# Performance work log

Hardware: AMD Instinct MI355X
Metric: run time of the kernel (lower is better)

Reference implementation:

```python
import jax, jax.numpy as jnp
import numpy as np

B, L, S, H = 2, 256, 384, 768
Tc, Dc = 16, 50
WV, WD = 20000, 100
CV = 128
NEG = -1e30


def _lstm_scan(x, Wih, Whh, bih, bhh):
    # x: [N, T, D] -> hs: [N, T, Hc]; torch LSTM gate order i,f,g,o
    N = x.shape[0]
    Hc = Whh.shape[1]
    h0 = jnp.zeros((N, Hc), x.dtype)

    def step(carry, xt):
        h, c = carry
        g = xt @ Wih.T + h @ Whh.T + bih + bhh  # [N, 4Hc]
        i, f, gg, o = jnp.split(g, 4, axis=-1)
        i = jax.nn.sigmoid(i)
        f = jax.nn.sigmoid(f)
        gg = jnp.tanh(gg)
        o = jax.nn.sigmoid(o)
        c = f * c + i * gg
        h = o * jnp.tanh(c)
        return (h, c), h

    _, hs = jax.lax.scan(step, (h0, h0), jnp.swapaxes(x, 0, 1))
    return jnp.swapaxes(hs, 0, 1)


def setup_inputs() -> dict:
    key = jax.random.key(0)
    ks = jax.random.split(key, 10)
    bert_emb = jax.random.normal(ks[0], (B, S, H), jnp.float32)
    pieces2word = jax.random.randint(ks[1], (B, L, S), 0, 2, jnp.int32)
    word_ids = jax.random.randint(ks[2], (B, L), 0, WV, jnp.int32)
    char_count = jax.random.randint(ks[3], (B, L), 1, Tc + 1, jnp.int32)
    char_ids = jax.random.randint(ks[4], (B, L, Tc), 0, CV, jnp.int32)
    # mask consistent with ragged char lengths (first char_count positions valid)
    token_masks_char = (jnp.arange(Tc)[None, None, :] < char_count[..., None]).astype(jnp.int32)
    word_table = jax.random.normal(ks[5], (WV, WD), jnp.float32) * 0.02
    char_table = jax.random.normal(ks[6], (CV, Dc), jnp.float32) * 0.02
    sc = 1.0 / np.sqrt(Dc)

    def lstm_w(k):
        a, b, c, d = jax.random.split(k, 4)
        return (jax.random.uniform(a, (4 * Dc, Dc), jnp.float32, -sc, sc),
                jax.random.uniform(b, (4 * Dc, Dc), jnp.float32, -sc, sc),
                jax.random.uniform(c, (4 * Dc,), jnp.float32, -sc, sc),
                jax.random.uniform(d, (4 * Dc,), jnp.float32, -sc, sc))

    Wih_f, Whh_f, bih_f, bhh_f = lstm_w(ks[7])
    Wih_b, Whh_b, bih_b, bhh_b = lstm_w(ks[8])
    return dict(bert_emb=bert_emb, pieces2word=pieces2word, word_ids=word_ids,
                char_count=char_count, char_ids=char_ids, token_masks_char=token_masks_char,
                word_table=word_table, char_table=char_table,
                Wih_f=Wih_f, Whh_f=Whh_f, bih_f=bih_f, bhh_f=bhh_f,
                Wih_b=Wih_b, Whh_b=Whh_b, bih_b=bih_b, bhh_b=bhh_b)


def reference(bert_emb, pieces2word, word_ids, char_count, char_ids, token_masks_char,
              word_table, char_table, Wih_f, Whh_f, bih_f, bhh_f, Wih_b, Whh_b, bih_b, bhh_b):
    # --- piece2word max pool (expand + masked_fill(min) + max over pieces) ---
    minv = jnp.min(bert_emb)
    # [B, L, S, H] intermediate, as in the original expand
    masked = jnp.where(pieces2word[..., None] != 0, bert_emb[:, None, :, :], minv)
    word_reps = jnp.max(masked, axis=2)  # [B, L, H]
    # dropouts are identity in eval mode

    # --- word embedding lookup ---
    word_embed = word_table[word_ids]  # [B, L, WD]

    # --- char bi-LSTM with packed-sequence semantics ---
    lens = jnp.maximum(char_count.reshape(-1), 1)  # char_count[char_count==0]=1
    x = char_table[char_ids.reshape(B * L, Tc)]  # [N, Tc, Dc]
    h_fwd = _lstm_scan(x, Wih_f, Whh_f, bih_f, bhh_f)
    # reverse each sequence within its valid length for the backward direction
    t = jnp.arange(Tc)[None, :]
    idx = jnp.where(t < lens[:, None], lens[:, None] - 1 - t, t)  # [N, Tc]
    x_rev = jnp.take_along_axis(x, idx[..., None], axis=1)
    h_bwd = _lstm_scan(x_rev, Wih_b, Whh_b, bih_b, bhh_b)
    h_bwd = jnp.take_along_axis(h_bwd, idx[..., None], axis=1)  # back to original order
    h = jnp.concatenate([h_fwd, h_bwd], axis=-1)  # [N, Tc, 2*Dc]
    valid = (t < lens[:, None])[..., None]
    h = jnp.where(valid, h, 0.0)  # pad_packed_sequence zero-pads beyond length
    h = h.reshape(B, L, Tc, 2 * Dc)

    # --- combine(..., 'max'): masked max over ragged char groups ---
    m = jnp.where(token_masks_char[..., None] == 0, NEG, 0.0)
    sup = jnp.max(m + h, axis=2)  # [B, L, 2*Dc]
    sup = jnp.where(sup == NEG, 0.0, sup)

    return jnp.concatenate([word_reps, word_embed, sup], axis=-1)  # [B, L, H+WD+2*Dc]
```

## Files before the change

kernel.cpp:

```cpp
#include <hip/hip_runtime.h>
#include <float.h>

#define Bb 2
#define Ll 256
#define Ss 384
#define Hh 768
#define Tc 16
#define Dc 50
#define WD 100
#define CV 128
#define NG 200
#define OUTC 968


__device__ inline float tanh_fast(float x) {
    float e = __expf(2.f * x);
    return 1.f - 2.f / (e + 1.f);
}
__device__ inline float sigmoid_fast(float x) {
    return 1.f / (1.f + __expf(-x));
}


__global__ __launch_bounds__(256) void prep_kernel(
        const float* __restrict__ bert, const float* __restrict__ char_table,
        const float* __restrict__ Wih_f, const float* __restrict__ bih_f, const float* __restrict__ bhh_f,
        const float* __restrict__ Wih_b, const float* __restrict__ bih_b, const float* __restrict__ bhh_b,
        const int* __restrict__ word_ids, const float* __restrict__ word_table,
        float* __restrict__ minp, float* __restrict__ xpt, float* __restrict__ out) {
    int blk = blockIdx.x, tid = threadIdx.x;
    if (blk < 256) {
        const int n = Bb * Ss * Hh;
        float m = FLT_MAX;
        for (int i = blk * 256 + tid; i < n; i += 256 * 256) m = fminf(m, bert[i]);
        #pragma unroll
        for (int off = 32; off; off >>= 1) m = fminf(m, __shfl_down(m, off, 64));
        __shared__ float red[4];
        if ((tid & 63) == 0) red[tid >> 6] = m;
        __syncthreads();
        if (tid == 0) minp[blk] = fminf(fminf(red[0], red[1]), fminf(red[2], red[3]));
    } else if (blk < 272) {
        int idx = blk - 256;
        int dir = idx >> 3, c0 = (idx & 7) * 16;
        const float* Wih = dir ? Wih_b : Wih_f;
        const float* bih = dir ? bih_b : bih_f;
        const float* bhh = dir ? bhh_b : bhh_f;
        __shared__ float ct[16][Dc];
        for (int e = tid; e < 16 * Dc; e += 256)
            ((float*)ct)[e] = char_table[c0 * Dc + e];
        __syncthreads();
        if (tid < NG) {
            float w[Dc];
            #pragma unroll
            for (int j = 0; j < Dc; j++) w[j] = Wih[tid * Dc + j];
            float bias = bih[tid] + bhh[tid];
            for (int cid = 0; cid < 16; cid++) {
                float a = bias;
                #pragma unroll
                for (int j = 0; j < Dc; j++) a += w[j] * ct[cid][j];
                xpt[(dir * CV + c0 + cid) * NG + tid] = a;
            }
        }
    } else {
        for (int i = (blk - 272) * 256 + tid; i < Bb * Ll * WD; i += 64 * 256) {
            int bl = i / WD, d = i - bl * WD;
            out[(size_t)bl * OUTC + Hh + d] = word_table[(size_t)word_ids[bl] * WD + d];
        }
    }
}


#define LT 8

__global__ __launch_bounds__(256) void word_kernel(
        const float* __restrict__ bert, const int* __restrict__ p2w,
        const float* __restrict__ minp, float* __restrict__ out) {
    int tid = threadIdx.x;
    __shared__ float sminv;
    __shared__ float sacc[4][LT][128];
    if (tid < 64) {
        float m = fminf(fminf(minp[tid], minp[tid + 64]),
                        fminf(minp[tid + 128], minp[tid + 192]));
        #pragma unroll
        for (int off = 32; off; off >>= 1) m = fminf(m, __shfl_down(m, off, 64));
        if (tid == 0) sminv = m;
    }
    int blk = blockIdx.x;
    int hc = blk % 6;
    int lt = (blk / 6) & 31;
    int b  = blk / 192;
    int l0 = lt * LT;
    int w    = tid >> 6;
    int lane = tid & 63;

    const float2* bb2 = (const float2*)(bert + (size_t)b * Ss * Hh + hc * 128);
    const int*    pm  = p2w + ((size_t)b * Ll + l0) * Ss;

    float2 acc[LT];
    #pragma unroll
    for (int r = 0; r < LT; r++) { acc[r].x = -FLT_MAX; acc[r].y = -FLT_MAX; }

    int s0 = w * 96;
    for (int s = s0; s < s0 + 96; s += 4) {
        float2 v0 = bb2[(size_t)(s + 0) * 384 + lane];
        float2 v1 = bb2[(size_t)(s + 1) * 384 + lane];
        float2 v2 = bb2[(size_t)(s + 2) * 384 + lane];
        float2 v3 = bb2[(size_t)(s + 3) * 384 + lane];
        #pragma unroll
        for (int r = 0; r < LT; r++) {
            const int* pr = pm + r * Ss + s;
            if (pr[0]) { acc[r].x = fmaxf(acc[r].x, v0.x); acc[r].y = fmaxf(acc[r].y, v0.y); }
            if (pr[1]) { acc[r].x = fmaxf(acc[r].x, v1.x); acc[r].y = fmaxf(acc[r].y, v1.y); }
            if (pr[2]) { acc[r].x = fmaxf(acc[r].x, v2.x); acc[r].y = fmaxf(acc[r].y, v2.y); }
            if (pr[3]) { acc[r].x = fmaxf(acc[r].x, v3.x); acc[r].y = fmaxf(acc[r].y, v3.y); }
        }
    }
    #pragma unroll
    for (int r = 0; r < LT; r++)
        *(float2*)&sacc[w][r][lane * 2] = acc[r];
    __syncthreads();

    float mv = sminv;
    #pragma unroll
    for (int e = tid; e < LT * 128; e += 256) {
        int r = e >> 7, c = e & 127;
        float m0 = fmaxf(sacc[0][r][c], sacc[1][r][c]);
        float m1 = fmaxf(sacc[2][r][c], sacc[3][r][c]);
        float m  = fmaxf(m0, m1);
        if (m == -FLT_MAX) m = mv;
        out[((size_t)(b * Ll + l0 + r)) * OUTC + hc * 128 + c] = m;
    }
}


__global__ __launch_bounds__(256) void lstm_kernel(
        const int* __restrict__ char_ids, const int* __restrict__ char_count,
        const float* __restrict__ Whh_f, const float* __restrict__ Whh_b,
        const float* __restrict__ xpt, float* __restrict__ out) {
    int n = blockIdx.x, dir = blockIdx.y, tid = threadIdx.x;
    const float* Whh = dir ? Whh_b : Whh_f;

    __shared__ float xg[Tc][NG];
    __shared__ float gs[NG];
    __shared__ __align__(16) float hs[52];
    __shared__ int scid[Tc];

    int len = char_count[n];
    if (len < 1) len = 1;
    if (tid < Tc) {
        int t = tid;
        int st = dir ? (t < len ? len - 1 - t : t) : t;
        scid[t] = char_ids[n * Tc + st];
    }
    if (tid < 52) hs[tid] = 0.f;
    __syncthreads();

    for (int e = tid; e < Tc * NG; e += 256) {
        int t = e / NG, g = e - t * NG;
        xg[t][g] = xpt[(dir * CV + scid[t]) * NG + g];
    }
    float w[52];
    if (tid < NG) {
        #pragma unroll
        for (int j = 0; j < Dc; j++) w[j] = Whh[tid * Dc + j];
        w[50] = 0.f; w[51] = 0.f;
    }
    __syncthreads();

    float c = 0.f, maxv = -FLT_MAX;
    for (int t = 0; t < Tc; t++) {
        if (tid < NG) {
            float g = xg[t][tid];
            #pragma unroll
            for (int j = 0; j < 52; j += 4) {
                float4 hv = *(const float4*)&hs[j];
                g += hv.x * w[j] + hv.y * w[j+1] + hv.z * w[j+2] + hv.w * w[j+3];
            }
            gs[tid] = g;
        }
        __syncthreads();
        if (tid < Dc) {
            float si = sigmoid_fast(gs[tid]);
            float sf = sigmoid_fast(gs[tid + 50]);
            float tg = tanh_fast(gs[tid + 100]);
            float so = sigmoid_fast(gs[tid + 150]);
            c = sf * c + si * tg;
            float h = so * tanh_fast(c);
            hs[tid] = h;
            if (t < len) maxv = fmaxf(maxv, h);
        }
        __syncthreads();
    }
    if (tid < Dc)
        out[(size_t)n * OUTC + (Hh + WD) + dir * Dc + tid] = maxv;
}

extern "C" void kernel_launch(void* const* d_in, const int* in_sizes, int n_in,
                              void* d_out, int out_size, void* d_ws, size_t ws_size,
                              hipStream_t stream) {
    const float* bert       = (const float*)d_in[0];
    const int*   p2w        = (const int*)d_in[1];
    const int*   word_ids   = (const int*)d_in[2];
    const int*   char_count = (const int*)d_in[3];
    const int*   char_ids   = (const int*)d_in[4];
    const float* word_table = (const float*)d_in[6];
    const float* char_table = (const float*)d_in[7];
    const float* Wih_f = (const float*)d_in[8];
    const float* Whh_f = (const float*)d_in[9];
    const float* bih_f = (const float*)d_in[10];
    const float* bhh_f = (const float*)d_in[11];
    const float* Wih_b = (const float*)d_in[12];
    const float* Whh_b = (const float*)d_in[13];
    const float* bih_b = (const float*)d_in[14];
    const float* bhh_b = (const float*)d_in[15];
    float* out = (float*)d_out;

    float* minp = (float*)d_ws;
    float* xpt  = minp + 256;

    prep_kernel<<<336, 256, 0, stream>>>(
        bert, char_table, Wih_f, bih_f, bhh_f, Wih_b, bih_b, bhh_b,
        word_ids, word_table, minp, xpt, out);
    word_kernel<<<384, 256, 0, stream>>>(bert, p2w, minp, out);
    lstm_kernel<<<dim3(512, 2), 256, 0, stream>>>(
        char_ids, char_count, Whh_f, Whh_b, xpt, out);
}
```

Measured before the change: 146.9 us.

## Precompute pieces2word as bitmasks and use six waves in word max-pool

```diff
diff --git a/kernel.cpp b/kernel.cpp
--- a/kernel.cpp
+++ b/kernel.cpp
@@ -11,6 +11,7 @@
 #define CV 128
 #define NG 200
 #define OUTC 968
+#define NW 6
 
 
 __device__ inline float tanh_fast(float x) {
@@ -27,7 +28,9 @@
         const float* __restrict__ Wih_f, const float* __restrict__ bih_f, const float* __restrict__ bhh_f,
         const float* __restrict__ Wih_b, const float* __restrict__ bih_b, const float* __restrict__ bhh_b,
         const int* __restrict__ word_ids, const float* __restrict__ word_table,
-        float* __restrict__ minp, float* __restrict__ xpt, float* __restrict__ out) {
+        const int* __restrict__ p2w,
+        float* __restrict__ minp, float* __restrict__ xpt,
+        unsigned long long* __restrict__ pmask, float* __restrict__ out) {
     int blk = blockIdx.x, tid = threadIdx.x;
     if (blk < 256) {
         const int n = Bb * Ss * Hh;
@@ -61,23 +64,32 @@
                 xpt[(dir * CV + c0 + cid) * NG + tid] = a;
             }
         }
-    } else {
+    } else if (blk < 336) {
         for (int i = (blk - 272) * 256 + tid; i < Bb * Ll * WD; i += 64 * 256) {
             int bl = i / WD, d = i - bl * WD;
             out[(size_t)bl * OUTC + Hh + d] = word_table[(size_t)word_ids[bl] * WD + d];
         }
+    } else {
+        int gw   = (blk - 336) * 4 + (tid >> 6);
+        int lane = tid & 63;
+        for (int k = 0; k < 64; k++) {
+            int W = gw * 64 + k;
+            int v = p2w[(size_t)W * 64 + lane];
+            unsigned long long bm = __ballot(v != 0);
+            if (lane == 0) pmask[W] = bm;
+        }
     }
 }
 
 
 #define LT 8
 
-__global__ __launch_bounds__(256) void word_kernel(
-        const float* __restrict__ bert, const int* __restrict__ p2w,
+__global__ __launch_bounds__(384) void word_kernel(
+        const float* __restrict__ bert, const unsigned long long* __restrict__ pmask,
         const float* __restrict__ minp, float* __restrict__ out) {
     int tid = threadIdx.x;
     __shared__ float sminv;
-    __shared__ float sacc[4][LT][128];
+    __shared__ float sacc[NW][LT][128];
     if (tid < 64) {
         float m = fminf(fminf(minp[tid], minp[tid + 64]),
                         fminf(minp[tid + 128], minp[tid + 192]));
@@ -93,26 +105,31 @@
     int w    = tid >> 6;
     int lane = tid & 63;
 
-    const float2* bb2 = (const float2*)(bert + (size_t)b * Ss * Hh + hc * 128);
-    const int*    pm  = p2w + ((size_t)b * Ll + l0) * Ss;
+    unsigned mlo[LT], mhi[LT];
+    #pragma unroll
+    for (int r = 0; r < LT; r++) {
+        unsigned long long mw = pmask[(size_t)(b * Ll + l0 + r) * NW + w];
+        mlo[r] = __builtin_amdgcn_readfirstlane((unsigned)mw);
+        mhi[r] = __builtin_amdgcn_readfirstlane((unsigned)(mw >> 32));
+    }
+
+    const float2* bb2 = (const float2*)(bert + (size_t)b * Ss * Hh) + hc * 64 + lane;
 
     float2 acc[LT];
     #pragma unroll
     for (int r = 0; r < LT; r++) { acc[r].x = -FLT_MAX; acc[r].y = -FLT_MAX; }
 
-    int s0 = w * 96;
-    for (int s = s0; s < s0 + 96; s += 4) {
-        float2 v0 = bb2[(size_t)(s + 0) * 384 + lane];
-        float2 v1 = bb2[(size_t)(s + 1) * 384 + lane];
-        float2 v2 = bb2[(size_t)(s + 2) * 384 + lane];
-        float2 v3 = bb2[(size_t)(s + 3) * 384 + lane];
+    int sbase = w * 64;
+    #pragma unroll 8
+    for (int j = 0; j < 64; j++) {
+        float2 v = bb2[(size_t)(sbase + j) * 384];
         #pragma unroll
         for (int r = 0; r < LT; r++) {
-            const int* pr = pm + r * Ss + s;
-            if (pr[0]) { acc[r].x = fmaxf(acc[r].x, v0.x); acc[r].y = fmaxf(acc[r].y, v0.y); }
-            if (pr[1]) { acc[r].x = fmaxf(acc[r].x, v1.x); acc[r].y = fmaxf(acc[r].y, v1.y); }
-            if (pr[2]) { acc[r].x = fmaxf(acc[r].x, v2.x); acc[r].y = fmaxf(acc[r].y, v2.y); }
-            if (pr[3]) { acc[r].x = fmaxf(acc[r].x, v3.x); acc[r].y = fmaxf(acc[r].y, v3.y); }
+            unsigned bit = (j < 32) ? (mlo[r] & (1u << j)) : (mhi[r] & (1u << (j - 32)));
+            if (bit) {
+                acc[r].x = fmaxf(acc[r].x, v.x);
+                acc[r].y = fmaxf(acc[r].y, v.y);
+            }
         }
     }
     #pragma unroll
@@ -121,12 +138,12 @@
     __syncthreads();
 
     float mv = sminv;
-    #pragma unroll
-    for (int e = tid; e < LT * 128; e += 256) {
+    for (int e = tid; e < LT * 128; e += 384) {
         int r = e >> 7, c = e & 127;
         float m0 = fmaxf(sacc[0][r][c], sacc[1][r][c]);
         float m1 = fmaxf(sacc[2][r][c], sacc[3][r][c]);
-        float m  = fmaxf(m0, m1);
+        float m2 = fmaxf(sacc[4][r][c], sacc[5][r][c]);
+        float m  = fmaxf(fmaxf(m0, m1), m2);
         if (m == -FLT_MAX) m = mv;
         out[((size_t)(b * Ll + l0 + r)) * OUTC + hc * 128 + c] = m;
     }
@@ -217,11 +234,12 @@
 
     float* minp = (float*)d_ws;
     float* xpt  = minp + 256;
-
-    prep_kernel<<<336, 256, 0, stream>>>(
+    unsigned long long* pmask = (unsigned long long*)(xpt + 2 * CV * NG);
+
+    prep_kernel<<<348, 256, 0, stream>>>(
         bert, char_table, Wih_f, bih_f, bhh_f, Wih_b, bih_b, bhh_b,
-        word_ids, word_table, minp, xpt, out);
-    word_kernel<<<384, 256, 0, stream>>>(bert, p2w, minp, out);
+        word_ids, word_table, p2w, minp, xpt, pmask, out);
+    word_kernel<<<384, 384, 0, stream>>>(bert, pmask, minp, out);
     lstm_kernel<<<dim3(512, 2), 256, 0, stream>>>(
         char_ids, char_count, Whh_f, Whh_b, xpt, out);
 }
```

Result: slower. 158.9 us (+8.2%).

## Split word max-pool over S into partials, fuse into prep and LSTM kernels

Applied to the files above, without the earlier changes.

```diff
diff --git a/kernel.cpp b/kernel.cpp
--- a/kernel.cpp
+++ b/kernel.cpp
@@ -11,6 +11,8 @@
 #define CV 128
 #define NG 200
 #define OUTC 968
+#define LT 8
+#define NSC 4
 
 
 __device__ inline float tanh_fast(float x) {
@@ -22,12 +24,14 @@
 }
 
 
-__global__ __launch_bounds__(256) void prep_kernel(
-        const float* __restrict__ bert, const float* __restrict__ char_table,
+__global__ __launch_bounds__(256) void kernelA(
+        const float* __restrict__ bert, const int* __restrict__ p2w,
+        const float* __restrict__ char_table,
         const float* __restrict__ Wih_f, const float* __restrict__ bih_f, const float* __restrict__ bhh_f,
         const float* __restrict__ Wih_b, const float* __restrict__ bih_b, const float* __restrict__ bhh_b,
         const int* __restrict__ word_ids, const float* __restrict__ word_table,
-        float* __restrict__ minp, float* __restrict__ xpt, float* __restrict__ out) {
+        float* __restrict__ minp, float* __restrict__ xpt, float* __restrict__ partial,
+        float* __restrict__ out) {
     int blk = blockIdx.x, tid = threadIdx.x;
     if (blk < 256) {
         const int n = Bb * Ss * Hh;
@@ -61,138 +65,147 @@
                 xpt[(dir * CV + c0 + cid) * NG + tid] = a;
             }
         }
-    } else {
+    } else if (blk < 336) {
         for (int i = (blk - 272) * 256 + tid; i < Bb * Ll * WD; i += 64 * 256) {
             int bl = i / WD, d = i - bl * WD;
             out[(size_t)bl * OUTC + Hh + d] = word_table[(size_t)word_ids[bl] * WD + d];
         }
+    } else {
+        int idx = blk - 336;
+        int hc  = idx % 6;
+        int lt  = (idx / 6) & 31;
+        int bsc = idx / 192;
+        int b   = bsc >> 2, sc = bsc & 3;
+        int w    = tid >> 6;
+        int lane = tid & 63;
+        int s0 = sc * 96 + w * 24;
+
+        const int* pm = p2w + ((size_t)(b * Ll + lt * LT)) * Ss + s0;
+        unsigned m[LT];
+        #pragma unroll
+        for (int r = 0; r < LT; r++) {
+            int v = (lane < 24) ? pm[r * Ss + lane] : 0;
+            unsigned long long bal = __ballot(v != 0);
+            m[r] = __builtin_amdgcn_readfirstlane((unsigned)bal);
+        }
+
+        const float2* bb2 = (const float2*)(bert + (size_t)b * Ss * Hh) + hc * 64 + lane;
+        float2 acc[LT];
+        #pragma unroll
+        for (int r = 0; r < LT; r++) { acc[r].x = -FLT_MAX; acc[r].y = -FLT_MAX; }
+
+        #pragma unroll
+        for (int j = 0; j < 24; j++) {
+            float2 v = bb2[(size_t)(s0 + j) * 384];
+            #pragma unroll
+            for (int r = 0; r < LT; r++) {
+                if (m[r] & (1u << j)) {
+                    acc[r].x = fmaxf(acc[r].x, v.x);
+                    acc[r].y = fmaxf(acc[r].y, v.y);
+                }
+            }
+        }
+
+        __shared__ float sacc[4][LT][128];
+        #pragma unroll
+        for (int r = 0; r < LT; r++)
+            *(float2*)&sacc[w][r][lane * 2] = acc[r];
+        __syncthreads();
+
+        for (int e = tid; e < LT * 128; e += 256) {
+            int r = e >> 7, c = e & 127;
+            float m0 = fmaxf(fmaxf(sacc[0][r][c], sacc[1][r][c]),
+                             fmaxf(sacc[2][r][c], sacc[3][r][c]));
+            size_t row = (size_t)b * Ll + lt * LT + r;
+            partial[((size_t)sc * (Bb * Ll) + row) * Hh + hc * 128 + c] = m0;
+        }
     }
 }
 
 
-#define LT 8
-
-__global__ __launch_bounds__(256) void word_kernel(
-        const float* __restrict__ bert, const int* __restrict__ p2w,
-        const float* __restrict__ minp, float* __restrict__ out) {
-    int tid = threadIdx.x;
-    __shared__ float sminv;
-    __shared__ float sacc[4][LT][128];
-    if (tid < 64) {
-        float m = fminf(fminf(minp[tid], minp[tid + 64]),
-                        fminf(minp[tid + 128], minp[tid + 192]));
-        #pragma unroll
-        for (int off = 32; off; off >>= 1) m = fminf(m, __shfl_down(m, off, 64));
-        if (tid == 0) sminv = m;
-    }
-    int blk = blockIdx.x;
-    int hc = blk % 6;
-    int lt = (blk / 6) & 31;
-    int b  = blk / 192;
-    int l0 = lt * LT;
-    int w    = tid >> 6;
-    int lane = tid & 63;
-
-    const float2* bb2 = (const float2*)(bert + (size_t)b * Ss * Hh + hc * 128);
-    const int*    pm  = p2w + ((size_t)b * Ll + l0) * Ss;
-
-    float2 acc[LT];
-    #pragma unroll
-    for (int r = 0; r < LT; r++) { acc[r].x = -FLT_MAX; acc[r].y = -FLT_MAX; }
-
-    int s0 = w * 96;
-    for (int s = s0; s < s0 + 96; s += 4) {
-        float2 v0 = bb2[(size_t)(s + 0) * 384 + lane];
-        float2 v1 = bb2[(size_t)(s + 1) * 384 + lane];
-        float2 v2 = bb2[(size_t)(s + 2) * 384 + lane];
-        float2 v3 = bb2[(size_t)(s + 3) * 384 + lane];
-        #pragma unroll
-        for (int r = 0; r < LT; r++) {
-            const int* pr = pm + r * Ss + s;
-            if (pr[0]) { acc[r].x = fmaxf(acc[r].x, v0.x); acc[r].y = fmaxf(acc[r].y, v0.y); }
-            if (pr[1]) { acc[r].x = fmaxf(acc[r].x, v1.x); acc[r].y = fmaxf(acc[r].y, v1.y); }
-            if (pr[2]) { acc[r].x = fmaxf(acc[r].x, v2.x); acc[r].y = fmaxf(acc[r].y, v2.y); }
-            if (pr[3]) { acc[r].x = fmaxf(acc[r].x, v3.x); acc[r].y = fmaxf(acc[r].y, v3.y); }
-        }
-    }
-    #pragma unroll
-    for (int r = 0; r < LT; r++)
-        *(float2*)&sacc[w][r][lane * 2] = acc[r];
-    __syncthreads();
-
-    float mv = sminv;
-    #pragma unroll
-    for (int e = tid; e < LT * 128; e += 256) {
-        int r = e >> 7, c = e & 127;
-        float m0 = fmaxf(sacc[0][r][c], sacc[1][r][c]);
-        float m1 = fmaxf(sacc[2][r][c], sacc[3][r][c]);
-        float m  = fmaxf(m0, m1);
-        if (m == -FLT_MAX) m = mv;
-        out[((size_t)(b * Ll + l0 + r)) * OUTC + hc * 128 + c] = m;
-    }
-}
-
-
-__global__ __launch_bounds__(256) void lstm_kernel(
+__global__ __launch_bounds__(256) void kernelB(
         const int* __restrict__ char_ids, const int* __restrict__ char_count,
         const float* __restrict__ Whh_f, const float* __restrict__ Whh_b,
-        const float* __restrict__ xpt, float* __restrict__ out) {
-    int n = blockIdx.x, dir = blockIdx.y, tid = threadIdx.x;
-    const float* Whh = dir ? Whh_b : Whh_f;
-
-    __shared__ float xg[Tc][NG];
-    __shared__ float gs[NG];
-    __shared__ __align__(16) float hs[52];
-    __shared__ int scid[Tc];
-
-    int len = char_count[n];
-    if (len < 1) len = 1;
-    if (tid < Tc) {
-        int t = tid;
-        int st = dir ? (t < len ? len - 1 - t : t) : t;
-        scid[t] = char_ids[n * Tc + st];
+        const float* __restrict__ xpt, const float* __restrict__ partial,
+        const float* __restrict__ minp, float* __restrict__ out) {
+    int blk = blockIdx.x, tid = threadIdx.x;
+    if (blk < 1024) {
+        int n = blk >> 1, dir = blk & 1;
+        const float* Whh = dir ? Whh_b : Whh_f;
+
+        __shared__ float xg[Tc][NG];
+        __shared__ float gs[NG];
+        __shared__ __align__(16) float hs[52];
+        __shared__ int scid[Tc];
+
+        int len = char_count[n];
+        if (len < 1) len = 1;
+        if (tid < Tc) {
+            int t = tid;
+            int st = dir ? (t < len ? len - 1 - t : t) : t;
+            scid[t] = char_ids[n * Tc + st];
+        }
+        if (tid < 52) hs[tid] = 0.f;
+        __syncthreads();
+
+        for (int e = tid; e < Tc * NG; e += 256) {
+            int t = e / NG, g = e - t * NG;
+            xg[t][g] = xpt[(dir * CV + scid[t]) * NG + g];
+        }
+        float w[52];
+        if (tid < NG) {
+            #pragma unroll
+            for (int j = 0; j < Dc; j++) w[j] = Whh[tid * Dc + j];
+            w[50] = 0.f; w[51] = 0.f;
+        }
+        __syncthreads();
+
+        float c = 0.f, maxv = -FLT_MAX;
+        for (int t = 0; t < Tc; t++) {
+            if (tid < NG) {
+                float g = xg[t][tid];
+                #pragma unroll
+                for (int j = 0; j < 52; j += 4) {
+                    float4 hv = *(const float4*)&hs[j];
+                    g += hv.x * w[j] + hv.y * w[j+1] + hv.z * w[j+2] + hv.w * w[j+3];
+                }
+                gs[tid] = g;
+            }
+            __syncthreads();
+            if (tid < Dc) {
+                float si = sigmoid_fast(gs[tid]);
+                float sf = sigmoid_fast(gs[tid + 50]);
+                float tg = tanh_fast(gs[tid + 100]);
+                float so = sigmoid_fast(gs[tid + 150]);
+                c = sf * c + si * tg;
+                float h = so * tanh_fast(c);
+                hs[tid] = h;
+                if (t < len) maxv = fmaxf(maxv, h);
+            }
+            __syncthreads();
+        }
+        if (tid < Dc)
+            out[(size_t)n * OUTC + (Hh + WD) + dir * Dc + tid] = maxv;
+    } else {
+        __shared__ float sminv;
+        if (tid < 64) {
+            float m = fminf(fminf(minp[tid], minp[tid + 64]),
+                            fminf(minp[tid + 128], minp[tid + 192]));
+            #pragma unroll
+            for (int off = 32; off; off >>= 1) m = fminf(m, __shfl_down(m, off, 64));
+            if (tid == 0) sminv = m;
+        }
+        __syncthreads();
+        float mv = sminv;
+        const int TOT = Bb * Ll * Hh;
+        for (int e = (blk - 1024) * 256 + tid; e < TOT; e += 384 * 256) {
+            float m = fmaxf(fmaxf(partial[e], partial[TOT + e]),
+                            fmaxf(partial[2 * TOT + e], partial[3 * TOT + e]));
+            if (m == -FLT_MAX) m = mv;
+            int row = e / Hh, c = e - row * Hh;
+            out[(size_t)row * OUTC + c] = m;
+        }
     }
-    if (tid < 52) hs[tid] = 0.f;
-    __syncthreads();
-
-    for (int e = tid; e < Tc * NG; e += 256) {
-        int t = e / NG, g = e - t * NG;
-        xg[t][g] = xpt[(dir * CV + scid[t]) * NG + g];
-    }
-    float w[52];
-    if (tid < NG) {
-        #pragma unroll
-        for (int j = 0; j < Dc; j++) w[j] = Whh[tid * Dc + j];
-        w[50] = 0.f; w[51] = 0.f;
-    }
-    __syncthreads();
-
-    float c = 0.f, maxv = -FLT_MAX;
-    for (int t = 0; t < Tc; t++) {
-        if (tid < NG) {
-            float g = xg[t][tid];
-            #pragma unroll
-            for (int j = 0; j < 52; j += 4) {
-                float4 hv = *(const float4*)&hs[j];
-                g += hv.x * w[j] + hv.y * w[j+1] + hv.z * w[j+2] + hv.w * w[j+3];
-            }
-            gs[tid] = g;
-        }
-        __syncthreads();
-        if (tid < Dc) {
-            float si = sigmoid_fast(gs[tid]);
-            float sf = sigmoid_fast(gs[tid + 50]);
-            float tg = tanh_fast(gs[tid + 100]);
-            float so = sigmoid_fast(gs[tid + 150]);
-            c = sf * c + si * tg;
-            float h = so * tanh_fast(c);
-            hs[tid] = h;
-            if (t < len) maxv = fmaxf(maxv, h);
-        }
-        __syncthreads();
-    }
-    if (tid < Dc)
-        out[(size_t)n * OUTC + (Hh + WD) + dir * Dc + tid] = maxv;
 }
 
 extern "C" void kernel_launch(void* const* d_in, const int* in_sizes, int n_in,
@@ -215,13 +228,13 @@
     const float* bhh_b = (const float*)d_in[15];
     float* out = (float*)d_out;
 
-    float* minp = (float*)d_ws;
-    float* xpt  = minp + 256;
-
-    prep_kernel<<<336, 256, 0, stream>>>(
-        bert, char_table, Wih_f, bih_f, bhh_f, Wih_b, bih_b, bhh_b,
-        word_ids, word_table, minp, xpt, out);
-    word_kernel<<<384, 256, 0, stream>>>(bert, p2w, minp, out);
-    lstm_kernel<<<dim3(512, 2), 256, 0, stream>>>(
-        char_ids, char_count, Whh_f, Whh_b, xpt, out);
-}
+    float* minp    = (float*)d_ws;
+    float* xpt     = minp + 256;
+    float* partial = xpt + 2 * CV * NG;
+
+    kernelA<<<1872, 256, 0, stream>>>(
+        bert, p2w, char_table, Wih_f, bih_f, bhh_f, Wih_b, bih_b, bhh_b,
+        word_ids, word_table, minp, xpt, partial, out);
+    kernelB<<<1408, 256, 0, stream>>>(
+        char_ids, char_count, Whh_f, Whh_b, xpt, partial, minp, out);
+}
```

Result: faster. 130.1 us (-11.4%).

## Merge word-max and LSTM kernels into one launch with ballot-packed masks

Applied to the files above, without the earlier changes.

```diff
diff --git a/kernel.cpp b/kernel.cpp
--- a/kernel.cpp
+++ b/kernel.cpp
@@ -22,25 +22,29 @@
 }
 
 
-__global__ __launch_bounds__(256) void prep_kernel(
+__global__ __launch_bounds__(256) void kernel1(
         const float* __restrict__ bert, const float* __restrict__ char_table,
         const float* __restrict__ Wih_f, const float* __restrict__ bih_f, const float* __restrict__ bhh_f,
         const float* __restrict__ Wih_b, const float* __restrict__ bih_b, const float* __restrict__ bhh_b,
         const int* __restrict__ word_ids, const float* __restrict__ word_table,
         float* __restrict__ minp, float* __restrict__ xpt, float* __restrict__ out) {
     int blk = blockIdx.x, tid = threadIdx.x;
-    if (blk < 256) {
-        const int n = Bb * Ss * Hh;
+    if (blk < 128) {
+        const int n4 = (Bb * Ss * Hh) / 4;
+        const float4* b4 = (const float4*)bert;
         float m = FLT_MAX;
-        for (int i = blk * 256 + tid; i < n; i += 256 * 256) m = fminf(m, bert[i]);
+        for (int i = blk * 256 + tid; i < n4; i += 128 * 256) {
+            float4 v = b4[i];
+            m = fminf(m, fminf(fminf(v.x, v.y), fminf(v.z, v.w)));
+        }
         #pragma unroll
         for (int off = 32; off; off >>= 1) m = fminf(m, __shfl_down(m, off, 64));
         __shared__ float red[4];
         if ((tid & 63) == 0) red[tid >> 6] = m;
         __syncthreads();
         if (tid == 0) minp[blk] = fminf(fminf(red[0], red[1]), fminf(red[2], red[3]));
-    } else if (blk < 272) {
-        int idx = blk - 256;
+    } else if (blk < 144) {
+        int idx = blk - 128;
         int dir = idx >> 3, c0 = (idx & 7) * 16;
         const float* Wih = dir ? Wih_b : Wih_f;
         const float* bih = dir ? bih_b : bih_f;
@@ -62,7 +66,7 @@
             }
         }
     } else {
-        for (int i = (blk - 272) * 256 + tid; i < Bb * Ll * WD; i += 64 * 256) {
+        for (int i = (blk - 144) * 256 + tid; i < Bb * Ll * WD; i += 64 * 256) {
             int bl = i / WD, d = i - bl * WD;
             out[(size_t)bl * OUTC + Hh + d] = word_table[(size_t)word_ids[bl] * WD + d];
         }
@@ -70,129 +74,141 @@
 }
 
 
-#define LT 8
-
-__global__ __launch_bounds__(256) void word_kernel(
+__global__ __launch_bounds__(256) void kernel2(
+        const int* __restrict__ char_ids, const int* __restrict__ char_count,
+        const float* __restrict__ Whh_f, const float* __restrict__ Whh_b,
+        const float* __restrict__ xpt,
         const float* __restrict__ bert, const int* __restrict__ p2w,
         const float* __restrict__ minp, float* __restrict__ out) {
-    int tid = threadIdx.x;
-    __shared__ float sminv;
-    __shared__ float sacc[4][LT][128];
-    if (tid < 64) {
-        float m = fminf(fminf(minp[tid], minp[tid + 64]),
-                        fminf(minp[tid + 128], minp[tid + 192]));
-        #pragma unroll
-        for (int off = 32; off; off >>= 1) m = fminf(m, __shfl_down(m, off, 64));
-        if (tid == 0) sminv = m;
+    __shared__ __align__(16) char smem[13888];
+    int blk = blockIdx.x, tid = threadIdx.x;
+
+    if (blk < 1024) {
+        float (*xg)[NG] = (float (*)[NG])smem;
+        float* gs  = (float*)(smem + 12800);
+        float* hs  = (float*)(smem + 13600);
+        int*   scid = (int*)(smem + 13808);
+
+        int n = blk >> 1, dir = blk & 1;
+        const float* Whh = dir ? Whh_b : Whh_f;
+
+        int len = char_count[n];
+        if (len < 1) len = 1;
+        if (tid < Tc) {
+            int t = tid;
+            int st = dir ? (t < len ? len - 1 - t : t) : t;
+            scid[t] = char_ids[n * Tc + st];
+        }
+        if (tid < 52) hs[tid] = 0.f;
+        __syncthreads();
+
+        for (int e = tid; e < Tc * (NG / 4); e += 256) {
+            int t = e / 50, q = e - t * 50;
+            ((float4*)xg[t])[q] = ((const float4*)&xpt[(dir * CV + scid[t]) * NG])[q];
+        }
+        float w[52];
+        if (tid < NG) {
+            #pragma unroll
+            for (int j = 0; j < Dc; j++) w[j] = Whh[tid * Dc + j];
+            w[50] = 0.f; w[51] = 0.f;
+        }
+        __syncthreads();
+
+        float c = 0.f, maxv = -FLT_MAX;
+        for (int t = 0; t < Tc; t++) {
+            if (tid < NG) {
+                float g = xg[t][tid];
+                #pragma unroll
+                for (int j = 0; j < 52; j += 4) {
+                    float4 hv = *(const float4*)&hs[j];
+                    g += hv.x * w[j] + hv.y * w[j+1] + hv.z * w[j+2] + hv.w * w[j+3];
+                }
+                gs[tid] = g;
+            }
+            __syncthreads();
+            if (tid < Dc) {
+                float si = sigmoid_fast(gs[tid]);
+                float sf = sigmoid_fast(gs[tid + 50]);
+                float tg = tanh_fast(gs[tid + 100]);
+                float so = sigmoid_fast(gs[tid + 150]);
+                c = sf * c + si * tg;
+                float h = so * tanh_fast(c);
+                hs[tid] = h;
+                if (t < len) maxv = fmaxf(maxv, h);
+            }
+            __syncthreads();
+        }
+        if (tid < Dc)
+            out[(size_t)n * OUTC + (Hh + WD) + dir * Dc + tid] = maxv;
+    } else {
+        float (*sacc)[4][128] = (float (*)[4][128])smem;
+        float* sminv = (float*)(smem + 8192);
+
+        if (tid < 64) {
+            float m = fminf(minp[tid], minp[tid + 64]);
+            #pragma unroll
+            for (int off = 32; off; off >>= 1) m = fminf(m, __shfl_down(m, off, 64));
+            if (tid == 0) *sminv = m;
+        }
+        int idx = blk - 1024;
+        int hc  = idx % 6;
+        int lt  = (idx / 6) & 63;
+        int b   = idx / 384;
+        int l0  = lt * 4;
+        int w    = tid >> 6;
+        int lane = tid & 63;
+        int s0 = w * 96;
+
+        const int* pm = p2w + ((size_t)(b * Ll + l0)) * Ss + s0;
+        unsigned m0[4], m1[4], m2[4];
+        #pragma unroll
+        for (int r = 0; r < 4; r++) {
+            unsigned long long b0 = __ballot(pm[r * Ss + lane] != 0);
+            unsigned long long b1 = __ballot(lane < 32 ? (pm[r * Ss + 64 + lane] != 0) : false);
+            m0[r] = __builtin_amdgcn_readfirstlane((unsigned)b0);
+            m1[r] = __builtin_amdgcn_readfirstlane((unsigned)(b0 >> 32));
+            m2[r] = __builtin_amdgcn_readfirstlane((unsigned)b1);
+        }
+
+        const float2* bb2 = (const float2*)(bert + (size_t)b * Ss * Hh) + hc * 64 + lane;
+        float2 acc[4];
+        #pragma unroll
+        for (int r = 0; r < 4; r++) { acc[r].x = -FLT_MAX; acc[r].y = -FLT_MAX; }
+
+        for (int jo = 0; jo < 96; jo += 8) {
+            float2 v[8];
+            #pragma unroll
+            for (int k = 0; k < 8; k++) v[k] = bb2[(size_t)(s0 + jo + k) * 384];
+            #pragma unroll
+            for (int k = 0; k < 8; k++) {
+                int j = jo + k;
+                #pragma unroll
+                for (int r = 0; r < 4; r++) {
+                    unsigned bit = (j < 32 ? m0[r] >> j
+                                 : j < 64 ? m1[r] >> (j - 32)
+                                          : m2[r] >> (j - 64)) & 1u;
+                    if (bit) {
+                        acc[r].x = fmaxf(acc[r].x, v[k].x);
+                        acc[r].y = fmaxf(acc[r].y, v[k].y);
+                    }
+                }
+            }
+        }
+        #pragma unroll
+        for (int r = 0; r < 4; r++)
+            *(float2*)&sacc[w][r][lane * 2] = acc[r];
+        __syncthreads();
+
+        float mv = *sminv;
+        #pragma unroll
+        for (int e = tid; e < 4 * 128; e += 256) {
+            int r = e >> 7, cx = e & 127;
+            float m = fmaxf(fmaxf(sacc[0][r][cx], sacc[1][r][cx]),
+                            fmaxf(sacc[2][r][cx], sacc[3][r][cx]));
+            if (m == -FLT_MAX) m = mv;
+            out[((size_t)(b * Ll + l0 + r)) * OUTC + hc * 128 + cx] = m;
+        }
     }
-    int blk = blockIdx.x;
-    int hc = blk % 6;
-    int lt = (blk / 6) & 31;
-    int b  = blk / 192;
-    int l0 = lt * LT;
-    int w    = tid >> 6;
-    int lane = tid & 63;
-
-    const float2* bb2 = (const float2*)(bert + (size_t)b * Ss * Hh + hc * 128);
-    const int*    pm  = p2w + ((size_t)b * Ll + l0) * Ss;
-
-    float2 acc[LT];
-    #pragma unroll
-    for (int r = 0; r < LT; r++) { acc[r].x = -FLT_MAX; acc[r].y = -FLT_MAX; }
-
-    int s0 = w * 96;
-    for (int s = s0; s < s0 + 96; s += 4) {
-        float2 v0 = bb2[(size_t)(s + 0) * 384 + lane];
-        float2 v1 = bb2[(size_t)(s + 1) * 384 + lane];
-        float2 v2 = bb2[(size_t)(s + 2) * 384 + lane];
-        float2 v3 = bb2[(size_t)(s + 3) * 384 + lane];
-        #pragma unroll
-        for (int r = 0; r < LT; r++) {
-            const int* pr = pm + r * Ss + s;
-            if (pr[0]) { acc[r].x = fmaxf(acc[r].x, v0.x); acc[r].y = fmaxf(acc[r].y, v0.y); }
-            if (pr[1]) { acc[r].x = fmaxf(acc[r].x, v1.x); acc[r].y = fmaxf(acc[r].y, v1.y); }
-            if (pr[2]) { acc[r].x = fmaxf(acc[r].x, v2.x); acc[r].y = fmaxf(acc[r].y, v2.y); }
-            if (pr[3]) { acc[r].x = fmaxf(acc[r].x, v3.x); acc[r].y = fmaxf(acc[r].y, v3.y); }
-        }
-    }
-    #pragma unroll
-    for (int r = 0; r < LT; r++)
-        *(float2*)&sacc[w][r][lane * 2] = acc[r];
-    __syncthreads();
-
-    float mv = sminv;
-    #pragma unroll
-    for (int e = tid; e < LT * 128; e += 256) {
-        int r = e >> 7, c = e & 127;
-        float m0 = fmaxf(sacc[0][r][c], sacc[1][r][c]);
-        float m1 = fmaxf(sacc[2][r][c], sacc[3][r][c]);
-        float m  = fmaxf(m0, m1);
-        if (m == -FLT_MAX) m = mv;
-        out[((size_t)(b * Ll + l0 + r)) * OUTC + hc * 128 + c] = m;
-    }
-}
-
-
-__global__ __launch_bounds__(256) void lstm_kernel(
-        const int* __restrict__ char_ids, const int* __restrict__ char_count,
-        const float* __restrict__ Whh_f, const float* __restrict__ Whh_b,
-        const float* __restrict__ xpt, float* __restrict__ out) {
-    int n = blockIdx.x, dir = blockIdx.y, tid = threadIdx.x;
-    const float* Whh = dir ? Whh_b : Whh_f;
-
-    __shared__ float xg[Tc][NG];
-    __shared__ float gs[NG];
-    __shared__ __align__(16) float hs[52];
-    __shared__ int scid[Tc];
-
-    int len = char_count[n];
-    if (len < 1) len = 1;
-    if (tid < Tc) {
-        int t = tid;
-        int st = dir ? (t < len ? len - 1 - t : t) : t;
-        scid[t] = char_ids[n * Tc + st];
-    }
-    if (tid < 52) hs[tid] = 0.f;
-    __syncthreads();
-
-    for (int e = tid; e < Tc * NG; e += 256) {
-        int t = e / NG, g = e - t * NG;
-        xg[t][g] = xpt[(dir * CV + scid[t]) * NG + g];
-    }
-    float w[52];
-    if (tid < NG) {
-        #pragma unroll
-        for (int j = 0; j < Dc; j++) w[j] = Whh[tid * Dc + j];
-        w[50] = 0.f; w[51] = 0.f;
-    }
-    __syncthreads();
-
-    float c = 0.f, maxv = -FLT_MAX;
-    for (int t = 0; t < Tc; t++) {
-        if (tid < NG) {
-            float g = xg[t][tid];
-            #pragma unroll
-            for (int j = 0; j < 52; j += 4) {
-                float4 hv = *(const float4*)&hs[j];
-                g += hv.x * w[j] + hv.y * w[j+1] + hv.z * w[j+2] + hv.w * w[j+3];
-            }
-            gs[tid] = g;
-        }
-        __syncthreads();
-        if (tid < Dc) {
-            float si = sigmoid_fast(gs[tid]);
-            float sf = sigmoid_fast(gs[tid + 50]);
-            float tg = tanh_fast(gs[tid + 100]);
-            float so = sigmoid_fast(gs[tid + 150]);
-            c = sf * c + si * tg;
-            float h = so * tanh_fast(c);
-            hs[tid] = h;
-            if (t < len) maxv = fmaxf(maxv, h);
-        }
-        __syncthreads();
-    }
-    if (tid < Dc)
-        out[(size_t)n * OUTC + (Hh + WD) + dir * Dc + tid] = maxv;
 }
 
 extern "C" void kernel_launch(void* const* d_in, const int* in_sizes, int n_in,
@@ -216,12 +232,11 @@
     float* out = (float*)d_out;
 
     float* minp = (float*)d_ws;
-    float* xpt  = minp + 256;
-
-    prep_kernel<<<336, 256, 0, stream>>>(
+    float* xpt  = minp + 128;
+
+    kernel1<<<208, 256, 0, stream>>>(
         bert, char_table, Wih_f, bih_f, bhh_f, Wih_b, bih_b, bhh_b,
         word_ids, word_table, minp, xpt, out);
-    word_kernel<<<384, 256, 0, stream>>>(bert, p2w, minp, out);
-    lstm_kernel<<<dim3(512, 2), 256, 0, stream>>>(
-        char_ids, char_count, Whh_f, Whh_b, xpt, out);
-}
+    kernel2<<<1792, 256, 0, stream>>>(
+        char_ids, char_count, Whh_f, Whh_b, xpt, bert, p2w, minp, out);
+}
```

Measured after the change: 123.4 us. -16.0%, faster.
